# Kernel tuning notes

Hardware: AMD Instinct MI355X
Metric: run time of the kernel (lower is better)

## Reference

```python
import jax, jax.numpy as jnp
import numpy as np

CH = 1280
HEADS = 8
HEAD_DIM = 160
INNER = HEADS * HEAD_DIM  # 1280


def setup_inputs() -> dict:
    key = jax.random.key(0)
    ks = jax.random.split(key, 6)
    s = 1.0 / np.sqrt(CH)
    return {
        "hidden_states": jax.random.normal(ks[0], (2, 4096, CH), dtype=jnp.float32),
        "w_q": jax.random.normal(ks[1], (CH, INNER), dtype=jnp.float32) * s,
        "w_k": jax.random.normal(ks[2], (CH, INNER), dtype=jnp.float32) * s,
        "w_v": jax.random.normal(ks[3], (CH, INNER), dtype=jnp.float32) * s,
        "w_out": jax.random.normal(ks[4], (INNER, CH), dtype=jnp.float32) * (1.0 / np.sqrt(INNER)),
        "b_out": jax.random.normal(ks[5], (CH,), dtype=jnp.float32) * 0.01,
    }


def reference(hidden_states, w_q, w_k, w_v, w_out, b_out):
    B, S, C = hidden_states.shape
    scale = 1.0 / np.sqrt(HEAD_DIM)
    # self-attention: context = hidden_states
    q = (hidden_states @ w_q).reshape(B, S, HEADS, HEAD_DIM)
    k = (hidden_states @ w_k).reshape(B, S, HEADS, HEAD_DIM)
    v = (hidden_states @ w_v).reshape(B, S, HEADS, HEAD_DIM)
    # [B, H, S, S] explicit score matrix (matches original non-flash path)
    scores = jnp.einsum("bqhd,bkhd->bhqk", q, k) * scale
    attn = jax.nn.softmax(scores, axis=-1)
    out = jnp.einsum("bhqk,bkhd->bqhd", attn, v).reshape(B, S, INNER)
    return out @ w_out + b_out
```

## Files before the change

### kernel.cpp

```cpp
#include <hip/hip_runtime.h>
#include <hip/hip_bf16.h>
#include <stdint.h>


using bf16x8 = __attribute__((ext_vector_type(8))) short;
using f32x4  = __attribute__((ext_vector_type(4))) float;

__device__ __forceinline__ short f2bf(float f) {
    union { float f; uint32_t u; } v; v.f = f;
    uint32_t r = v.u + 0x7fffu + ((v.u >> 16) & 1u);
    return (short)(r >> 16);
}

__device__ __forceinline__ void async16(const short* g, short* l) {
    __builtin_amdgcn_global_load_lds(
        (const __attribute__((address_space(1))) void*)g,
        (__attribute__((address_space(3))) void*)l, 16, 0, 0);
}

__global__ __launch_bounds__(256) void cast_hs(
    const float* __restrict__ hs, short* __restrict__ out)
{
    int i = (blockIdx.x * 256 + threadIdx.x) * 4;
    float4 v = *(const float4*)&hs[i];
    short4 s; s.x = f2bf(v.x); s.y = f2bf(v.y); s.z = f2bf(v.z); s.w = f2bf(v.w);
    *(short4*)&out[i] = s;
}

__global__ __launch_bounds__(256) void transpose_w(
    const float* __restrict__ w0, const float* __restrict__ w1,
    const float* __restrict__ w2, const float* __restrict__ w3,
    short* __restrict__ wqkvT, short* __restrict__ woutT)
{
    __shared__ float tile[32][33];
    int z = blockIdx.z;
    const float* src = (z == 0) ? w0 : (z == 1) ? w1 : (z == 2) ? w2 : w3;
    short* dst = (z == 3) ? woutT : (wqkvT + (long)z * 1280 * 1280);
    int k0 = blockIdx.x * 32, n0 = blockIdx.y * 32;
    int t = threadIdx.x, r = t >> 5, c = t & 31;
#pragma unroll
    for (int i = 0; i < 4; i++)
        tile[r + i * 8][c] = src[(long)(k0 + r + i * 8) * 1280 + n0 + c];
    __syncthreads();
#pragma unroll
    for (int i = 0; i < 4; i++)
        dst[(long)(n0 + r + i * 8) * 1280 + k0 + c] = f2bf(tile[c][r + i * 8]);
}

__global__ __launch_bounds__(256) void transpose_v(
    const short* __restrict__ v, short* __restrict__ vt)
{
    __shared__ short tile[32][33];
    int s0 = blockIdx.x * 32, d0 = blockIdx.y * 32;
    long bh = blockIdx.z;
    const short* src = v + bh * 4096 * 160;
    short* dst = vt + bh * 160 * 4096;
    int t = threadIdx.x, r = t >> 5, c = t & 31;
#pragma unroll
    for (int i = 0; i < 4; i++)
        tile[r + i * 8][c] = src[(s0 + r + i * 8) * 160 + d0 + c];
    __syncthreads();
#pragma unroll
    for (int i = 0; i < 4; i++)
        dst[(d0 + r + i * 8) * 4096 + s0 + c] = tile[c][r + i * 8];
}

template <int MODE>
__global__ __launch_bounds__(256, 3) void gemm_k(
    const short* __restrict__ A, const short* __restrict__ BT,
    short* __restrict__ q_h, short* __restrict__ k_h, short* __restrict__ v_h,
    float* __restrict__ outp, const float* __restrict__ bias)
{
    __shared__ __align__(16) short A_lds[128 * 64];
    __shared__ __align__(16) short B_lds[128 * 64];

    int t = threadIdx.x, wave = t >> 6, lane = t & 63;
    int quad = lane >> 4, l15 = lane & 15, h7 = l15 & 7;
    int wr = wave >> 1, wc = wave & 1;
    int m0 = blockIdx.y * 128, n0 = blockIdx.x * 128;

    f32x4 acc[4][4] = {};

    for (int kt = 0; kt < 1280; kt += 64) {
        __syncthreads();
#pragma unroll
        for (int i = 0; i < 4; i++) {
            int chunk = wave * 4 + i;
            int c = chunk * 64 + lane;
            int row = c >> 3, j = (c & 7) ^ (row & 7);
            async16(A  + (long)(m0 + row) * 1280 + kt + j * 8, A_lds + chunk * 512);
            async16(BT + (long)(n0 + row) * 1280 + kt + j * 8, B_lds + chunk * 512);
        }
        __syncthreads();

#pragma unroll
        for (int dk = 0; dk < 2; dk++) {
            bf16x8 a[4], b[4];
#pragma unroll
            for (int mi = 0; mi < 4; mi++) {
                int row = wr * 64 + mi * 16 + l15;
                a[mi] = *(const bf16x8*)&A_lds[row * 64 + ((dk * 4 + quad) ^ h7) * 8];
            }
#pragma unroll
            for (int ni = 0; ni < 4; ni++) {
                int row = wc * 64 + ni * 16 + l15;
                b[ni] = *(const bf16x8*)&B_lds[row * 64 + ((dk * 4 + quad) ^ h7) * 8];
            }
#pragma unroll
            for (int mi = 0; mi < 4; mi++)
#pragma unroll
                for (int ni = 0; ni < 4; ni++)
                    acc[mi][ni] = __builtin_amdgcn_mfma_f32_16x16x32_bf16(
                        a[mi], b[ni], acc[mi][ni], 0, 0, 0);
        }
    }

    const float SL2E = 0.07905694150420949f * 1.4426950408889634f;
#pragma unroll
    for (int mi = 0; mi < 4; mi++) {
#pragma unroll
        for (int ni = 0; ni < 4; ni++) {
#pragma unroll
            for (int r = 0; r < 4; r++) {
                int gr = m0 + wr * 64 + mi * 16 + quad * 4 + r;
                int gc = n0 + wc * 64 + ni * 16 + l15;
                float val = acc[mi][ni][r];
                if (MODE == 0) {
                    int which = gc / 1280;
                    int c1 = gc - which * 1280;
                    int hh = c1 / 160, d = c1 - hh * 160;
                    int b_ = gr >> 12, s = gr & 4095;
                    long addr = (((long)(b_ * 8 + hh)) * 4096 + s) * 160 + d;
                    if (which == 0) val *= SL2E;
                    short* dst = (which == 0) ? q_h : (which == 1) ? k_h : v_h;
                    dst[addr] = f2bf(val);
                } else {
                    outp[(long)gr * 1280 + gc] = val + bias[gc];
                }
            }
        }
    }
}

__global__ __launch_bounds__(256, 2) void flash_k(
    const short* __restrict__ q_h, const short* __restrict__ k_h,
    const short* __restrict__ v_t, short* __restrict__ attn_out)
{
    __shared__ __align__(16) short Ks128[64 * 128];
    __shared__ __align__(16) short Ks32 [64 * 32];
    __shared__ __align__(16) short Vs   [176 * 64];
    __shared__ __align__(16) short Ps   [128 * 72];

    int t = threadIdx.x, wave = t >> 6, lane = t & 63;
    int quad = lane >> 4, l15 = lane & 15, h7 = l15 & 7;
    int qt = blockIdx.x;
    long bh = blockIdx.y;
    int b = (int)(bh >> 3), h = (int)(bh & 7);

    bf16x8 qf[2][5];
#pragma unroll
    for (int mi = 0; mi < 2; mi++) {
        const short* qg = q_h + (bh * 4096 + qt * 128 + wave * 32 + mi * 16 + l15) * 160;
#pragma unroll
        for (int dk = 0; dk < 5; dk++)
            qf[mi][dk] = *(const bf16x8*)&qg[dk * 32 + quad * 8];
    }
    {
        short v1 = (t < 16) ? (short)0x3F80 : (short)0;
        short4 s4 = { v1, v1, v1, v1 };
        *(short4*)&Vs[160 * 64 + t * 4] = s4;
    }

    auto stageK = [&](int k0) {
        const short* kg = k_h + (bh * 4096 + k0) * 160;
#pragma unroll
        for (int i = 0; i < 4; i++) {
            int chunk = wave * 4 + i;
            int c = chunk * 64 + lane;
            int row = c >> 4, j = (c & 15) ^ (row & 7);
            async16(kg + row * 160 + j * 8, Ks128 + chunk * 512);
        }
        {
            int row = wave * 16 + (lane >> 2);
            int j = (lane & 3) ^ (row & 3);
            async16(kg + row * 160 + 128 + j * 8, Ks32 + wave * 512);
        }
    };
    auto stageV = [&](int k0) {
#pragma unroll
        for (int i = 0; i < 5; i++) {
            int chunk = wave * 5 + i;
            int c = chunk * 64 + lane;
            int row = c >> 3, j = (c & 7) ^ (row & 7);
            async16(v_t + (bh * 160 + row) * 4096 + k0 + j * 8, Vs + chunk * 512);
        }
    };

    f32x4 o[2][11] = {};

    stageK(0);
    stageV(0);
    asm volatile("s_waitcnt vmcnt(5)" ::: "memory");
    asm volatile("s_waitcnt lgkmcnt(0)" ::: "memory");
    __builtin_amdgcn_s_barrier();

    for (int k0 = 0; k0 < 4096; k0 += 64) {
#pragma unroll
        for (int nt = 0; nt < 4; nt++) {
            f32x4 s0 = {}, s1 = {};
#pragma unroll
            for (int dk = 0; dk < 4; dk++) {
                bf16x8 bk = *(const bf16x8*)
                    &Ks128[(nt * 16 + l15) * 128 + ((dk * 4 + quad) ^ h7) * 8];
                s0 = __builtin_amdgcn_mfma_f32_16x16x32_bf16(qf[0][dk], bk, s0, 0, 0, 0);
                s1 = __builtin_amdgcn_mfma_f32_16x16x32_bf16(qf[1][dk], bk, s1, 0, 0, 0);
            }
            {
                bf16x8 bk = *(const bf16x8*)
                    &Ks32[(nt * 16 + l15) * 32 + ((quad ^ (l15 & 3)) * 8)];
                s0 = __builtin_amdgcn_mfma_f32_16x16x32_bf16(qf[0][4], bk, s0, 0, 0, 0);
                s1 = __builtin_amdgcn_mfma_f32_16x16x32_bf16(qf[1][4], bk, s1, 0, 0, 0);
            }
#pragma unroll
            for (int r = 0; r < 4; r++) {
                int pr0 = (wave * 32 + quad * 4 + r) * 72 + nt * 16 + l15;
                Ps[pr0]            = f2bf(exp2f(s0[r] - 16.f));
                Ps[pr0 + 16 * 72]  = f2bf(exp2f(s1[r] - 16.f));
            }
        }

        asm volatile("s_waitcnt vmcnt(0)" ::: "memory");
        asm volatile("s_waitcnt lgkmcnt(0)" ::: "memory");
        __builtin_amdgcn_s_barrier();

        if (k0 + 64 < 4096) stageK(k0 + 64);

#pragma unroll
        for (int ks = 0; ks < 2; ks++) {
            bf16x8 ap0 = *(const bf16x8*)&Ps[(wave * 32 + l15) * 72 + ks * 32 + quad * 8];
            bf16x8 ap1 = *(const bf16x8*)&Ps[(wave * 32 + 16 + l15) * 72 + ks * 32 + quad * 8];
#pragma unroll
            for (int ct = 0; ct < 11; ct++) {
                int row = ct * 16 + l15;
                bf16x8 bv = *(const bf16x8*)&Vs[row * 64 + (((ks * 4 + quad) ^ (row & 7)) * 8)];
                o[0][ct] = __builtin_amdgcn_mfma_f32_16x16x32_bf16(ap0, bv, o[0][ct], 0, 0, 0);
                o[1][ct] = __builtin_amdgcn_mfma_f32_16x16x32_bf16(ap1, bv, o[1][ct], 0, 0, 0);
            }
        }

        asm volatile("s_waitcnt vmcnt(0)" ::: "memory");
        asm volatile("s_waitcnt lgkmcnt(0)" ::: "memory");
        __builtin_amdgcn_s_barrier();

        if (k0 + 64 < 4096) stageV(k0 + 64);
    }

#pragma unroll
    for (int mi = 0; mi < 2; mi++) {
        float inv[4];
#pragma unroll
        for (int r = 0; r < 4; r++)
            inv[r] = 1.0f / __shfl(o[mi][10][r], (lane & 48));
#pragma unroll
        for (int ct = 0; ct < 10; ct++)
#pragma unroll
            for (int r = 0; r < 4; r++) {
                int gr = b * 4096 + qt * 128 + wave * 32 + mi * 16 + quad * 4 + r;
                int gc = h * 160 + ct * 16 + l15;
                attn_out[(long)gr * 1280 + gc] = f2bf(o[mi][ct][r] * inv[r]);
            }
    }
}

extern "C" void kernel_launch(void* const* d_in, const int* in_sizes, int n_in,
                              void* d_out, int out_size, void* d_ws, size_t ws_size,
                              hipStream_t stream)
{
    const float* hs = (const float*)d_in[0];
    const float* wq = (const float*)d_in[1];
    const float* wk = (const float*)d_in[2];
    const float* wv = (const float*)d_in[3];
    const float* wo = (const float*)d_in[4];
    const float* bo = (const float*)d_in[5];
    float* out = (float*)d_out;

    char* ws = (char*)d_ws;
    short* wqkvT = (short*)(ws + 0);
    short* woutT = (short*)(ws + 9830400);
    short* q_h   = (short*)(ws + 13107200);
    short* k_h   = (short*)(ws + 34078720);
    short* v_t   = (short*)(ws + 55050240);
    short* v_h   = (short*)(ws + 76021760);
    short* attn  = v_h;
    short* hs_bf = v_t;

    cast_hs<<<10240, 256, 0, stream>>>(hs, hs_bf);
    transpose_w<<<dim3(40, 40, 4), 256, 0, stream>>>(wq, wk, wv, wo, wqkvT, woutT);
    gemm_k<0><<<dim3(30, 64), 256, 0, stream>>>(hs_bf, wqkvT, q_h, k_h, v_h,
                                                nullptr, nullptr);
    transpose_v<<<dim3(128, 5, 16), 256, 0, stream>>>(v_h, v_t);
    flash_k<<<dim3(32, 16), 256, 0, stream>>>(q_h, k_h, v_t, attn);
    gemm_k<1><<<dim3(10, 64), 256, 0, stream>>>(attn, woutT, nullptr, nullptr,
                                                nullptr, out, bo);
}
```

Baseline: 465.2 us.

## Switch flash attention to 32x32x16 MFMA with register row-sum accumulation

Reworks the flash attention kernel from 16x16x32 to 32x32x16 bf16 MFMA tiles. S is computed transposed as K·Q so each lane holds a full query column, and P is packed with v_cvt_pk_bf16_f32 into a swizzled LDS layout. The softmax denominator is now summed in registers from the rounded bf16 P values, replacing the extra ones-row in V, which removes one of eleven output tiles per wave. It also adds s_setprio around the MFMA loops and changes the Ks32 swizzle, at the cost of more complex lane-to-row mapping in the epilogue.

```diff
diff --git a/kernel.cpp b/kernel.cpp
--- a/kernel.cpp
+++ b/kernel.cpp
@@ -5,6 +5,7 @@
 
 using bf16x8 = __attribute__((ext_vector_type(8))) short;
 using f32x4  = __attribute__((ext_vector_type(4))) float;
+using f32x16 = __attribute__((ext_vector_type(16))) float;
 
 __device__ __forceinline__ short f2bf(float f) {
     union { float f; uint32_t u; } v; v.f = f;
@@ -148,27 +149,21 @@
 {
     __shared__ __align__(16) short Ks128[64 * 128];
     __shared__ __align__(16) short Ks32 [64 * 32];
-    __shared__ __align__(16) short Vs   [176 * 64];
+    __shared__ __align__(16) short Vs   [160 * 64];
     __shared__ __align__(16) short Ps   [128 * 72];
 
     int t = threadIdx.x, wave = t >> 6, lane = t & 63;
-    int quad = lane >> 4, l15 = lane & 15, h7 = l15 & 7;
+    int l31 = lane & 31, hi = lane >> 5;
     int qt = blockIdx.x;
     long bh = blockIdx.y;
     int b = (int)(bh >> 3), h = (int)(bh & 7);
 
-    bf16x8 qf[2][5];
-#pragma unroll
-    for (int mi = 0; mi < 2; mi++) {
-        const short* qg = q_h + (bh * 4096 + qt * 128 + wave * 32 + mi * 16 + l15) * 160;
-#pragma unroll
-        for (int dk = 0; dk < 5; dk++)
-            qf[mi][dk] = *(const bf16x8*)&qg[dk * 32 + quad * 8];
-    }
+    bf16x8 qf[10];
     {
-        short v1 = (t < 16) ? (short)0x3F80 : (short)0;
-        short4 s4 = { v1, v1, v1, v1 };
-        *(short4*)&Vs[160 * 64 + t * 4] = s4;
+        const short* qg = q_h + (bh * 4096 + qt * 128 + wave * 32 + l31) * 160;
+#pragma unroll
+        for (int dk = 0; dk < 10; dk++)
+            qf[dk] = *(const bf16x8*)&qg[dk * 16 + hi * 8];
     }
 
     auto stageK = [&](int k0) {
@@ -182,7 +177,7 @@
         }
         {
             int row = wave * 16 + (lane >> 2);
-            int j = (lane & 3) ^ (row & 3);
+            int j = (lane & 3) ^ ((lane >> 3) & 3);
             async16(kg + row * 160 + 128 + j * 8, Ks32 + wave * 512);
         }
     };
@@ -196,7 +191,8 @@
         }
     };
 
-    f32x4 o[2][11] = {};
+    f32x16 o[5] = {};
+    float lacc = 0.f;
 
     stageK(0);
     stageV(0);
@@ -204,28 +200,40 @@
     asm volatile("s_waitcnt lgkmcnt(0)" ::: "memory");
     __builtin_amdgcn_s_barrier();
 
+    int prow = (wave * 32 + l31) * 72;
+
     for (int k0 = 0; k0 < 4096; k0 += 64) {
 #pragma unroll
-        for (int nt = 0; nt < 4; nt++) {
-            f32x4 s0 = {}, s1 = {};
-#pragma unroll
-            for (int dk = 0; dk < 4; dk++) {
-                bf16x8 bk = *(const bf16x8*)
-                    &Ks128[(nt * 16 + l15) * 128 + ((dk * 4 + quad) ^ h7) * 8];
-                s0 = __builtin_amdgcn_mfma_f32_16x16x32_bf16(qf[0][dk], bk, s0, 0, 0, 0);
-                s1 = __builtin_amdgcn_mfma_f32_16x16x32_bf16(qf[1][dk], bk, s1, 0, 0, 0);
-            }
-            {
-                bf16x8 bk = *(const bf16x8*)
-                    &Ks32[(nt * 16 + l15) * 32 + ((quad ^ (l15 & 3)) * 8)];
-                s0 = __builtin_amdgcn_mfma_f32_16x16x32_bf16(qf[0][4], bk, s0, 0, 0, 0);
-                s1 = __builtin_amdgcn_mfma_f32_16x16x32_bf16(qf[1][4], bk, s1, 0, 0, 0);
-            }
-#pragma unroll
-            for (int r = 0; r < 4; r++) {
-                int pr0 = (wave * 32 + quad * 4 + r) * 72 + nt * 16 + l15;
-                Ps[pr0]            = f2bf(exp2f(s0[r] - 16.f));
-                Ps[pr0 + 16 * 72]  = f2bf(exp2f(s1[r] - 16.f));
+        for (int kt = 0; kt < 2; kt++) {
+            f32x16 s = {};
+            __builtin_amdgcn_s_setprio(1);
+#pragma unroll
+            for (int dk = 0; dk < 8; dk++) {
+                bf16x8 ka = *(const bf16x8*)
+                    &Ks128[(kt * 32 + l31) * 128 + (((dk * 2 + hi) ^ (l31 & 7)) * 8)];
+                s = __builtin_amdgcn_mfma_f32_32x32x16_bf16(ka, qf[dk], s, 0, 0, 0);
+            }
+#pragma unroll
+            for (int dk = 8; dk < 10; dk++) {
+                bf16x8 ka = *(const bf16x8*)
+                    &Ks32[(kt * 32 + l31) * 32 + ((((dk - 8) * 2 + hi) ^ ((l31 >> 1) & 3)) * 8)];
+                s = __builtin_amdgcn_mfma_f32_32x32x16_bf16(ka, qf[dk], s, 0, 0, 0);
+            }
+            __builtin_amdgcn_s_setprio(0);
+
+#pragma unroll
+            for (int rg = 0; rg < 4; rg++) {
+#pragma unroll
+                for (int c = 0; c < 2; c++) {
+                    float va = exp2f(s[rg * 4 + 2 * c]     - 16.f);
+                    float vb = exp2f(s[rg * 4 + 2 * c + 1] - 16.f);
+                    uint32_t pk;
+                    asm("v_cvt_pk_bf16_f32 %0, %1, %2" : "=v"(pk) : "v"(va), "v"(vb));
+                    lacc += __uint_as_float(pk << 16)
+                          + __uint_as_float(pk & 0xffff0000u);
+                    int so = (kt * 4 + rg) ^ (l31 & 7);
+                    *(uint32_t*)&Ps[prow + so * 8 + 2 * c + 4 * hi] = pk;
+                }
             }
         }
 
@@ -235,18 +243,20 @@
 
         if (k0 + 64 < 4096) stageK(k0 + 64);
 
-#pragma unroll
-        for (int ks = 0; ks < 2; ks++) {
-            bf16x8 ap0 = *(const bf16x8*)&Ps[(wave * 32 + l15) * 72 + ks * 32 + quad * 8];
-            bf16x8 ap1 = *(const bf16x8*)&Ps[(wave * 32 + 16 + l15) * 72 + ks * 32 + quad * 8];
-#pragma unroll
-            for (int ct = 0; ct < 11; ct++) {
-                int row = ct * 16 + l15;
-                bf16x8 bv = *(const bf16x8*)&Vs[row * 64 + (((ks * 4 + quad) ^ (row & 7)) * 8)];
-                o[0][ct] = __builtin_amdgcn_mfma_f32_16x16x32_bf16(ap0, bv, o[0][ct], 0, 0, 0);
-                o[1][ct] = __builtin_amdgcn_mfma_f32_16x16x32_bf16(ap1, bv, o[1][ct], 0, 0, 0);
-            }
-        }
+        __builtin_amdgcn_s_setprio(1);
+#pragma unroll
+        for (int ks = 0; ks < 4; ks++) {
+            bf16x8 ap = *(const bf16x8*)
+                &Ps[prow + (((2 * ks + hi) ^ (l31 & 7)) * 8)];
+#pragma unroll
+            for (int ct = 0; ct < 5; ct++) {
+                int row = ct * 32 + l31;
+                bf16x8 bv = *(const bf16x8*)
+                    &Vs[row * 64 + (((ks * 2 + hi) ^ (row & 7)) * 8)];
+                o[ct] = __builtin_amdgcn_mfma_f32_32x32x16_bf16(ap, bv, o[ct], 0, 0, 0);
+            }
+        }
+        __builtin_amdgcn_s_setprio(0);
 
         asm volatile("s_waitcnt vmcnt(0)" ::: "memory");
         asm volatile("s_waitcnt lgkmcnt(0)" ::: "memory");
@@ -255,21 +265,22 @@
         if (k0 + 64 < 4096) stageV(k0 + 64);
     }
 
-#pragma unroll
-    for (int mi = 0; mi < 2; mi++) {
-        float inv[4];
-#pragma unroll
-        for (int r = 0; r < 4; r++)
-            inv[r] = 1.0f / __shfl(o[mi][10][r], (lane & 48));
-#pragma unroll
-        for (int ct = 0; ct < 10; ct++)
-#pragma unroll
-            for (int r = 0; r < 4; r++) {
-                int gr = b * 4096 + qt * 128 + wave * 32 + mi * 16 + quad * 4 + r;
-                int gc = h * 160 + ct * 16 + l15;
-                attn_out[(long)gr * 1280 + gc] = f2bf(o[mi][ct][r] * inv[r]);
-            }
-    }
+    float lsum = lacc + __shfl_xor(lacc, 32);
+    float inv = 1.0f / lsum;
+    float iv[16];
+#pragma unroll
+    for (int r = 0; r < 16; r++)
+        iv[r] = __shfl(inv, (r & 3) + 8 * (r >> 2) + 4 * hi);
+
+#pragma unroll
+    for (int ct = 0; ct < 5; ct++)
+#pragma unroll
+        for (int r = 0; r < 16; r++) {
+            int crow = (r & 3) + 8 * (r >> 2) + 4 * hi;
+            int gr = b * 4096 + qt * 128 + wave * 32 + crow;
+            int gc = h * 160 + ct * 32 + l31;
+            attn_out[(long)gr * 1280 + gc] = f2bf(o[ct][r] * iv[r]);
+        }
 }
 
 extern "C" void kernel_launch(void* const* d_in, const int* in_sizes, int n_in,
```

After: 526.3 us. 1.13x slower.
